# Optimization experiments

Measured on AMD Instinct MI355X. Metric: run time of the kernel, lower is better.

## Reference

```python
import jax, jax.numpy as jnp
import numpy as np

D_LATENT = 128   # per-head dim AND input embedding dim (d_q default)
N_HEADS = 16
ROPE_BASE = 10000.0


def _rope(x):
    # x: [B, H, S, D]; interleaved-pair rotary embedding over seq axis (-2)
    B, H, S, D = x.shape
    half = D // 2
    inv_freq = 1.0 / (ROPE_BASE ** (jnp.arange(half, dtype=jnp.float32) * 2.0 / D))
    ang = jnp.arange(S, dtype=jnp.float32)[:, None] * inv_freq[None, :]  # [S, half]
    cos, sin = jnp.cos(ang), jnp.sin(ang)
    xp = x.reshape(B, H, S, half, 2)
    x0, x1 = xp[..., 0], xp[..., 1]
    r0 = x0 * cos - x1 * sin
    r1 = x1 * cos + x0 * sin
    return jnp.stack([r0, r1], axis=-1).reshape(B, H, S, D)


def setup_inputs() -> dict:
    key = jax.random.key(0)
    k_q, k_wq, k_wk, k_wv, k_wo = jax.random.split(key, 5)
    B, S, E = 2, 2048, D_LATENT
    inner = N_HEADS * D_LATENT
    sc_in = 1.0 / np.sqrt(E)
    sc_inner = 1.0 / np.sqrt(inner)
    return {
        "q": jax.random.normal(k_q, (B, S, E), dtype=jnp.float32),
        "W_q": jax.random.normal(k_wq, (E, inner), dtype=jnp.float32) * sc_in,
        "W_k": jax.random.normal(k_wk, (E, inner), dtype=jnp.float32) * sc_in,
        "W_v": jax.random.normal(k_wv, (E, inner), dtype=jnp.float32) * sc_in,
        "W_o": jax.random.normal(k_wo, (inner, E), dtype=jnp.float32) * sc_inner,
    }


def reference(q, W_q, W_k, W_v, W_o):
    B, S, E = q.shape
    H, D = N_HEADS, D_LATENT
    scale = 1.0 / np.sqrt(D)
    # projections -> [B, H, S, D]
    qh = (q @ W_q).reshape(B, S, H, D).transpose(0, 2, 1, 3)
    kh = (q @ W_k).reshape(B, S, H, D).transpose(0, 2, 1, 3)
    vh = (q @ W_v).reshape(B, S, H, D).transpose(0, 2, 1, 3)
    qh = _rope(qh)
    kh = _rope(kh)
    scores = jnp.einsum("bhsd,bhtd->bhst", qh, kh) * scale  # [B,H,S,S]
    causal = jnp.tril(jnp.ones((S, S), dtype=bool))
    scores = jnp.where(causal, scores, -jnp.inf)
    probs = jax.nn.softmax(scores, axis=-1)
    out = jnp.einsum("bhst,bhtd->bhsd", probs, vh)  # [B,H,S,D]
    out = out.transpose(0, 2, 1, 3).reshape(B, S, H * D)
    return out @ W_o
```

## Files before the change

kernel.cpp:

```cpp
#include <hip/hip_runtime.h>
#include <math.h>

#define S_LEN 2048
#define NH 16
#define DH 128
#define INNER 2048
#define NROWS 4096

typedef __attribute__((ext_vector_type(8))) short bf16x8;
typedef __attribute__((ext_vector_type(4))) float f32x4;

__device__ __forceinline__ short f2bf(float f) {
  union { float f; unsigned u; } v; v.f = f;
  unsigned r = (v.u + 0x7fffu + ((v.u >> 16) & 1u)) >> 16;
  return (short)(unsigned short)r;
}
__device__ __forceinline__ float bf2f(short s) {
  union { unsigned u; float f; } v; v.u = ((unsigned)(unsigned short)s) << 16;
  return v.f;
}
__device__ __forceinline__ int pkbf(float lo, float hi) {
  union { float f; unsigned u; } x, y;
  x.f = lo; y.f = hi;
  return (int)__builtin_amdgcn_perm(y.u + 0x8000u, x.u + 0x8000u, 0x07060302u);
}
__device__ __forceinline__ void gl2lds(const short* g, short* l) {
  __builtin_amdgcn_global_load_lds(
      (const __attribute__((address_space(1))) unsigned int*)g,
      (__attribute__((address_space(3))) unsigned int*)l, 16, 0, 0);
}

__global__ void k_prep(const float* __restrict__ X, const float* __restrict__ Wq,
                       const float* __restrict__ Wk, const float* __restrict__ Wv,
                       const float* __restrict__ Wo,
                       float* __restrict__ csT, short* __restrict__ Xbf,
                       short* __restrict__ WT, short* __restrict__ WoT,
                       float* __restrict__ outz) {
  const int bx = blockIdx.x, tid = threadIdx.x;
  if (bx < 512) {
    int idx = bx * 256 + tid;
    int i = idx & 63, s = idx >> 6;
    double invf = pow(10000.0, -(double)i / 64.0);
    float ang = (float)((double)s * invf);
    float sv, cv; sincosf(ang, &sv, &cv);
    csT[idx * 2] = cv; csT[idx * 2 + 1] = sv;
    return;
  }
  if (bx < 1024) {
    int idx = ((bx - 512) * 256 + tid) * 4;
    float4 xv = *(const float4*)&X[idx];
    short4 o; o.x = f2bf(xv.x); o.y = f2bf(xv.y); o.z = f2bf(xv.z); o.w = f2bf(xv.w);
    *(short4*)&Xbf[idx] = o;
    return;
  }
  if (bx >= 2048) {
    float4 z4 = make_float4(0.f, 0.f, 0.f, 0.f);
    ((float4*)outz)[(bx - 2048) * 512 + tid] = z4;
    ((float4*)outz)[(bx - 2048) * 512 + tid + 256] = z4;
    return;
  }
  __shared__ float tile[32][33];
  const float* src; short* dst; int R, C, c0, r0;
  if (bx < 1792) {
    int z = (bx - 1024) >> 8, t = (bx - 1024) & 255;
    src = (z == 0) ? Wq : ((z == 1) ? Wk : Wv);
    dst = WT + (size_t)z * INNER * 128; R = 128; C = INNER;
    c0 = (t & 63) * 32; r0 = (t >> 6) * 32;
  } else {
    int t = bx - 1792;
    src = Wo; dst = WoT; R = INNER; C = 128;
    c0 = (t & 3) * 32; r0 = (t >> 2) * 32;
  }
  int tx = tid & 31, ty = tid >> 5;
  #pragma unroll
  for (int dy = 0; dy < 32; dy += 8)
    tile[ty + dy][tx] = src[(size_t)(r0 + ty + dy) * C + c0 + tx];
  __syncthreads();
  #pragma unroll
  for (int dy = 0; dy < 32; dy += 8)
    dst[(size_t)(c0 + ty + dy) * R + r0 + tx] = f2bf(tile[tx][ty + dy]);
}

__global__ __launch_bounds__(256, 2) void k_qkv(
    const short* __restrict__ Xbf, const short* __restrict__ WT,
    const float* __restrict__ csT,
    short* __restrict__ Qg, short* __restrict__ Kg, short* __restrict__ Vg) {
  __shared__ __attribute__((aligned(16))) short As[128 * 136];
  __shared__ __attribute__((aligned(16))) short Bs[128 * 136];
  const int tid = threadIdx.x;
  const int n0 = blockIdx.x * 128, m0 = blockIdx.y * 128;
  for (int e = tid; e < 2048; e += 256)
    *(int4*)&As[(e >> 4) * 136 + (e & 15) * 8] =
        *(const int4*)&Xbf[(size_t)(m0 + (e >> 4)) * 128 + (e & 15) * 8];
  const int wid = tid >> 6, lane = tid & 63;
  const int l16 = lane & 15, quad = lane >> 4;
  const int wm = (wid & 1) * 64, wn = (wid >> 1) * 64;
  const int hh = n0 >> 7;
  const int bb = m0 >> 11, ss = m0 & 2047;
  const float qscale = 0.12751745f;
  for (int z = 0; z < 3; ++z) {
    __syncthreads();
    const short* Wp = WT + (size_t)z * INNER * 128;
    for (int e = tid; e < 2048; e += 256)
      *(int4*)&Bs[(e >> 4) * 136 + (e & 15) * 8] =
          *(const int4*)&Wp[(size_t)(n0 + (e >> 4)) * 128 + (e & 15) * 8];
    __syncthreads();
    f32x4 acc[4][4] = {};
    #pragma unroll
    for (int ks = 0; ks < 4; ++ks) {
      bf16x8 ax[4], bw[4];
      #pragma unroll
      for (int j = 0; j < 4; ++j) {
        ax[j] = *(const bf16x8*)&As[(wm + j * 16 + l16) * 136 + ks * 32 + quad * 8];
        bw[j] = *(const bf16x8*)&Bs[(wn + j * 16 + l16) * 136 + ks * 32 + quad * 8];
      }
      if (z < 2) {
        #pragma unroll
        for (int dt = 0; dt < 4; ++dt)
          #pragma unroll
          for (int st = 0; st < 4; ++st)
            acc[dt][st] = __builtin_amdgcn_mfma_f32_16x16x32_bf16(bw[dt], ax[st], acc[dt][st], 0, 0, 0);
      } else {
        #pragma unroll
        for (int mt = 0; mt < 4; ++mt)
          #pragma unroll
          for (int nt = 0; nt < 4; ++nt)
            acc[mt][nt] = __builtin_amdgcn_mfma_f32_16x16x32_bf16(ax[mt], bw[nt], acc[mt][nt], 0, 0, 0);
      }
    }
    if (z < 2) {
      __syncthreads();
      #pragma unroll
      for (int dt = 0; dt < 4; ++dt)
        #pragma unroll
        for (int st = 0; st < 4; ++st) {
          int d0 = wn + dt * 16 + quad * 4;
          int sl = wm + st * 16 + l16;
          int sg = ss + sl;
          float4 cs = *(const float4*)&csT[((size_t)sg * 64 + (d0 >> 1)) * 2];
          float x0 = acc[dt][st][0], x1 = acc[dt][st][1];
          float x2 = acc[dt][st][2], x3 = acc[dt][st][3];
          float r0 = x0 * cs.x - x1 * cs.y, r1 = x1 * cs.x + x0 * cs.y;
          float r2 = x2 * cs.z - x3 * cs.w, r3 = x3 * cs.z + x2 * cs.w;
          if (z == 0) { r0 *= qscale; r1 *= qscale; r2 *= qscale; r3 *= qscale; }
          int2 pk; pk.x = pkbf(r0, r1); pk.y = pkbf(r2, r3);
          *(int2*)&Bs[sl * 136 + d0] = pk;
        }
      __syncthreads();
      short* dst = (z == 0 ? Qg : Kg) + (((size_t)(bb * NH + hh)) * S_LEN + ss) * DH;
      #pragma unroll
      for (int it = 0; it < 8; ++it) {
        int u = tid + 256 * it;
        int row = u >> 4, c = u & 15;
        int cc = (z == 0) ? c : (c ^ (row & 15));
        *(int4*)&dst[(size_t)row * DH + cc * 8] = *(const int4*)&Bs[row * 136 + c * 8];
      }
    } else {
      __syncthreads();
      #pragma unroll
      for (int mt = 0; mt < 4; ++mt)
        #pragma unroll
        for (int nt = 0; nt < 4; ++nt) {
          int dl = wn + nt * 16 + l16;
          int sl = wm + mt * 16 + quad * 4;
          int2 pk;
          pk.x = pkbf(acc[mt][nt][0], acc[mt][nt][1]);
          pk.y = pkbf(acc[mt][nt][2], acc[mt][nt][3]);
          *(int2*)&As[dl * 136 + sl] = pk;
        }
      __syncthreads();
      #pragma unroll
      for (int rd = 0; rd < 8; ++rd) {
        int dl = (tid >> 4) + rd * 16;
        int sl = (tid & 15) * 8;
        int tile = (ss >> 6) + (sl >> 6);
        int tl = sl & 63;
        int ch = (tl >> 3) ^ (dl & 7);
        int4 vv = *(const int4*)&As[dl * 136 + sl];
        *(int4*)&Vg[(((size_t)(bb * NH + hh) * 32 + tile) * 128 + dl) * 64 + ch * 8] = vv;
      }
    }
  }
}

__global__ __launch_bounds__(256, 2) void k_attn(
    const short* __restrict__ Qg, const short* __restrict__ Kg,
    const short* __restrict__ Vt, short* __restrict__ Op,
    float* __restrict__ mlb) {
  __shared__ __attribute__((aligned(16))) short Ks[2][64 * 128];
  __shared__ __attribute__((aligned(16))) short Vs[2][128 * 64];
  __shared__ __attribute__((aligned(16))) short Ps[4][32 * 64];
  const int bid = blockIdx.x;
  const int bh = bid & 31, unit = bid >> 5;
  const int tid = threadIdx.x, wid = tid >> 6, lane = tid & 63;
  const int l16 = lane & 15, quad = lane >> 4, wq = wid * 32;
  const float CEXP2 = 23.083121f;
  const short* Qp = Qg + (size_t)bh * S_LEN * DH;
  const short* Kp = Kg + (size_t)bh * S_LEN * DH;
  const short* Vb = Vt + (size_t)bh * 32 * 8192;
  short* psw = &Ps[wid][0];
  int kcs[4], vcs[2];
  #pragma unroll
  for (int ks = 0; ks < 4; ++ks) kcs[ks] = ((ks * 4 + quad) ^ l16) * 8;
  #pragma unroll
  for (int ks = 0; ks < 2; ++ks) vcs[ks] = ((ks * 4 + quad) ^ (l16 & 7)) * 8;

  for (int seg = 0; seg < 2; ++seg) {
    const int qg = seg ? (15 - unit) : unit;
    const int par = seg;
    const int q0 = qg * 128, nj = qg + 1;
    __syncthreads();
    {
      const short* kg = Kp + (size_t)(par * 64) * DH;
      const short* vg = Vb + (size_t)par * 8192;
      #pragma unroll
      for (int i = 0; i < 4; ++i) {
        int sl = wid * 4 + i;
        gl2lds(kg + sl * 512 + lane * 8, &Ks[0][sl * 512]);
        gl2lds(vg + sl * 512 + lane * 8, &Vs[0][sl * 512]);
      }
    }
    bf16x8 qf[4][2];
    #pragma unroll
    for (int ks = 0; ks < 4; ++ks)
      #pragma unroll
      for (int qb = 0; qb < 2; ++qb)
        qf[ks][qb] = *(const bf16x8*)&Qp[(size_t)(q0 + wq + qb * 16 + l16) * DH +
                                         ks * 32 + quad * 8];
    float l_p[2] = {0.0f, 0.0f};
    f32x4 Oacc[8][2] = {};
    for (int jj = 0; jj < nj; ++jj) {
      const int b = jj & 1;
      __syncthreads();
      if (jj + 1 < nj) {
        const int jn = par + 2 * (jj + 1);
        const short* kg = Kp + (size_t)(jn * 64) * DH;
        const short* vg = Vb + (size_t)jn * 8192;
        #pragma unroll
        for (int i = 0; i < 4; ++i) {
          int sl = wid * 4 + i;
          gl2lds(kg + sl * 512 + lane * 8, &Ks[1 - b][sl * 512]);
          gl2lds(vg + sl * 512 + lane * 8, &Vs[1 - b][sl * 512]);
        }
      }
      f32x4 Sc[4][2] = {};
      #pragma unroll
      for (int ks = 0; ks < 4; ++ks) {
        bf16x8 kfr[4];
        #pragma unroll
        for (int nt = 0; nt < 4; ++nt)
          kfr[nt] = *(const bf16x8*)&Ks[b][(nt * 16 + l16) * 128 + kcs[ks]];
        #pragma unroll
        for (int nt = 0; nt < 4; ++nt)
          #pragma unroll
          for (int qb = 0; qb < 2; ++qb)
            Sc[nt][qb] = __builtin_amdgcn_mfma_f32_16x16x32_bf16(kfr[nt], qf[ks][qb],
                                                                 Sc[nt][qb], 0, 0, 0);
      }
      const int j = par + 2 * jj;
      if (jj == nj - 1) {
        #pragma unroll
        for (int nt = 0; nt < 4; ++nt)
          #pragma unroll
          for (int qb = 0; qb < 2; ++qb)
            #pragma unroll
            for (int r = 0; r < 4; ++r) {
              int tg = j * 64 + nt * 16 + quad * 4 + r;
              int qgl = q0 + wq + qb * 16 + l16;
              if (tg > qgl) Sc[nt][qb][r] = -1000.0f;
            }
      }
      #pragma unroll
      for (int qb = 0; qb < 2; ++qb) {
        float ls0 = 0.0f, ls1 = 0.0f;
        #pragma unroll
        for (int nt = 0; nt < 4; ++nt)
          #pragma unroll
          for (int r = 0; r < 4; ++r) {
            float pe = __builtin_amdgcn_exp2f(Sc[nt][qb][r] - CEXP2);
            Sc[nt][qb][r] = pe;
            if (nt & 1) ls1 += pe; else ls0 += pe;
          }
        l_p[qb] += ls0 + ls1;
        #pragma unroll
        for (int nt = 0; nt < 4; ++nt) {
          int2 pk;
          pk.x = pkbf(Sc[nt][qb][0], Sc[nt][qb][1]);
          pk.y = pkbf(Sc[nt][qb][2], Sc[nt][qb][3]);
          int ch = ((nt * 2 + (quad >> 1)) ^ (l16 & 7)) * 8 + (quad & 1) * 4;
          *(int2*)&psw[(qb * 16 + l16) * 64 + ch] = pk;
        }
      }
      #pragma unroll
      for (int ks = 0; ks < 2; ++ks) {
        bf16x8 vfr[8];
        #pragma unroll
        for (int nt = 0; nt < 8; ++nt)
          vfr[nt] = *(const bf16x8*)&Vs[b][(nt * 16 + l16) * 64 + vcs[ks]];
        bf16x8 bp[2];
        #pragma unroll
        for (int qb = 0; qb < 2; ++qb)
          bp[qb] = *(const bf16x8*)&psw[(qb * 16 + l16) * 64 + vcs[ks]];
        #pragma unroll
        for (int nt = 0; nt < 8; ++nt)
          #pragma unroll
          for (int qb = 0; qb < 2; ++qb)
            Oacc[nt][qb] = __builtin_amdgcn_mfma_f32_16x16x32_bf16(vfr[nt], bp[qb],
                                                                   Oacc[nt][qb], 0, 0, 0);
      }
    }
    __syncthreads();
    short* osl = &Ks[0][0] + wid * 4096;
    #pragma unroll
    for (int qb = 0; qb < 2; ++qb)
      #pragma unroll
      for (int nt = 0; nt < 8; ++nt) {
        int2 ov;
        ov.x = pkbf(Oacc[nt][qb][0], Oacc[nt][qb][1]);
        ov.y = pkbf(Oacc[nt][qb][2], Oacc[nt][qb][3]);
        int ch = ((nt * 2 + (quad >> 1)) ^ l16) * 8 + (quad & 1) * 4;
        *(int2*)&osl[(qb * 16 + l16) * 128 + ch] = ov;
      }
    size_t obase = ((size_t)(par * 32 + bh) * S_LEN + q0 + wq) * DH;
    #pragma unroll
    for (int it = 0; it < 8; ++it) {
      int u = lane + 64 * it;
      int row = u >> 4, c = u & 15;
      *(int4*)&Op[obase + (size_t)row * DH + c * 8] =
          *(const int4*)&osl[row * 128 + ((c ^ (row & 15)) * 8)];
    }
    #pragma unroll
    for (int qb = 0; qb < 2; ++qb) {
      float lt = l_p[qb];
      lt += __shfl_xor(lt, 16);
      lt += __shfl_xor(lt, 32);
      int qrow = q0 + wq + qb * 16 + l16;
      if (quad == 0)
        mlb[(size_t)(par * 32 + bh) * S_LEN + qrow] = lt;
    }
  }
}

__global__ __launch_bounds__(256, 2) void k_out(
    const short* __restrict__ Op, const float* __restrict__ mlb,
    const short* __restrict__ WoT, float* __restrict__ out) {
  __shared__ __attribute__((aligned(16))) short As[32 * 136];
  __shared__ __attribute__((aligned(16))) short Bs[128 * 136];
  __shared__ float cw[4][32];
  const int m0 = blockIdx.x * 32, h0 = blockIdx.y * 4;
  const int tid = threadIdx.x, wid = tid >> 6, lane = tid & 63;
  const int l16 = lane & 15, quad = lane >> 4;
  const int wm = (wid & 1) * 16, wn = (wid >> 1) * 64;
  if (tid < 128) {
    int rr = tid & 31, hh = tid >> 5;
    int row = m0 + rr, b = row >> 11, s = row & 2047;
    int bh = b * NH + h0 + hh;
    float l1 = mlb[(size_t)bh * S_LEN + s];
    float l2 = mlb[(size_t)(32 + bh) * S_LEN + s];
    cw[hh][rr] = 1.0f / (l1 + l2);
  }
  __syncthreads();
  f32x4 acc[4] = {};
  for (int hc = 0; hc < 4; ++hc) {
    int h = h0 + hc;
    #pragma unroll
    for (int it = 0; it < 4; ++it) {
      int e = tid + 256 * it;
      int rr = e >> 5, c4 = (e & 31) * 4;
      int row = m0 + rr, b = row >> 11, s = row & 2047;
      size_t base = ((size_t)(b * NH + h) * S_LEN + s) * DH + c4;
      short4 u1 = *(const short4*)&Op[base];
      short4 u2 = *(const short4*)&Op[(size_t)32 * S_LEN * DH + base];
      float c1 = cw[hc][rr];
      int2 o;
      o.x = pkbf(c1 * (bf2f(u1.x) + bf2f(u2.x)), c1 * (bf2f(u1.y) + bf2f(u2.y)));
      o.y = pkbf(c1 * (bf2f(u1.z) + bf2f(u2.z)), c1 * (bf2f(u1.w) + bf2f(u2.w)));
      *(int2*)&As[rr * 136 + c4] = o;
    }
    for (int e = tid; e < 2048; e += 256)
      *(int4*)&Bs[(e >> 4) * 136 + (e & 15) * 8] =
          *(const int4*)&WoT[(size_t)(e >> 4) * INNER + h * 128 + (e & 15) * 8];
    __syncthreads();
    #pragma unroll
    for (int ks = 0; ks < 4; ++ks) {
      bf16x8 a = *(const bf16x8*)&As[(wm + l16) * 136 + ks * 32 + quad * 8];
      bf16x8 b[4];
      #pragma unroll
      for (int nt = 0; nt < 4; ++nt)
        b[nt] = *(const bf16x8*)&Bs[(wn + nt * 16 + l16) * 136 + ks * 32 + quad * 8];
      #pragma unroll
      for (int nt = 0; nt < 4; ++nt)
        acc[nt] = __builtin_amdgcn_mfma_f32_16x16x32_bf16(a, b[nt], acc[nt], 0, 0, 0);
    }
    __syncthreads();
  }
  #pragma unroll
  for (int nt = 0; nt < 4; ++nt)
    #pragma unroll
    for (int r = 0; r < 4; ++r) {
      int gm = m0 + wm + quad * 4 + r;
      int gn = wn + nt * 16 + l16;
      atomicAdd(&out[(size_t)gm * 128 + gn], acc[nt][r]);
    }
}

extern "C" void kernel_launch(void* const* d_in, const int* in_sizes, int n_in,
                              void* d_out, int out_size, void* d_ws, size_t ws_size,
                              hipStream_t stream) {
  const float* q  = (const float*)d_in[0];
  const float* Wq = (const float*)d_in[1];
  const float* Wk = (const float*)d_in[2];
  const float* Wv = (const float*)d_in[3];
  const float* Wo = (const float*)d_in[4];
  float* out = (float*)d_out;
  char* ws = (char*)d_ws;
  const size_t MB = 1024 * 1024;
  float* csT = (float*)(ws + 0);
  short* WT  = (short*)(ws + 1 * MB);
  short* WoT = (short*)(ws + 2 * MB + 512 * 1024);
  short* Xbf = (short*)(ws + 3 * MB);
  short* Qg  = (short*)(ws + 8 * MB);
  short* Kg  = (short*)(ws + 24 * MB);
  short* Vg  = (short*)(ws + 40 * MB);
  short* Op  = (short*)(ws + 56 * MB);
  float* mlb = (float*)(ws + 88 * MB);

  k_prep<<<2304, 256, 0, stream>>>(q, Wq, Wk, Wv, Wo, csT, Xbf, WT, WoT, out);
  k_qkv<<<dim3(16, 32), 256, 0, stream>>>(Xbf, WT, csT, Qg, Kg, Vg);
  k_attn<<<512, 256, 0, stream>>>(Qg, Kg, Vg, Op, mlb);
  k_out<<<dim3(128, 4), 256, 0, stream>>>(Op, mlb, WoT, out);
}
```

Measured before the change: 158.4 us.

## Shuffle P fragments via permlane swaps, single-buffer V, raise attention occupancy

The P tile now goes from accumulator layout into MFMA operand layout through permlane32/permlane16 swaps held in registers, so the per-wave LDS scratch buffer and its stores and loads are gone. V is single-buffered and loaded at the start of each iteration, with explicit vmcnt waits and barriers before the PV matmul. The freed LDS lets launch bounds go to 3 blocks per SM. In exchange, V load latency is now exposed inside each iteration and the register cap tightens, which could cause spills.

New measurement: 169.1 us. 1.07x slower.

```diff
diff --git a/kernel.cpp b/kernel.cpp
--- a/kernel.cpp
+++ b/kernel.cpp
@@ -9,6 +9,7 @@
 
 typedef __attribute__((ext_vector_type(8))) short bf16x8;
 typedef __attribute__((ext_vector_type(4))) float f32x4;
+typedef __attribute__((ext_vector_type(2))) unsigned int u32x2;
 
 __device__ __forceinline__ short f2bf(float f) {
   union { float f; unsigned u; } v; v.f = f;
@@ -28,6 +29,14 @@
   __builtin_amdgcn_global_load_lds(
       (const __attribute__((address_space(1))) unsigned int*)g,
       (__attribute__((address_space(3))) unsigned int*)l, 16, 0, 0);
+}
+__device__ __forceinline__ void pl32swap(int& a, int& b) {
+  u32x2 r = __builtin_amdgcn_permlane32_swap((unsigned)a, (unsigned)b, false, false);
+  a = (int)r.x; b = (int)r.y;
+}
+__device__ __forceinline__ void pl16swap(int& a, int& b) {
+  u32x2 r = __builtin_amdgcn_permlane16_swap((unsigned)a, (unsigned)b, false, false);
+  a = (int)r.x; b = (int)r.y;
 }
 
 __global__ void k_prep(const float* __restrict__ X, const float* __restrict__ Wq,
@@ -183,13 +192,12 @@
   }
 }
 
-__global__ __launch_bounds__(256, 2) void k_attn(
+__global__ __launch_bounds__(256, 3) void k_attn(
     const short* __restrict__ Qg, const short* __restrict__ Kg,
     const short* __restrict__ Vt, short* __restrict__ Op,
     float* __restrict__ mlb) {
   __shared__ __attribute__((aligned(16))) short Ks[2][64 * 128];
-  __shared__ __attribute__((aligned(16))) short Vs[2][128 * 64];
-  __shared__ __attribute__((aligned(16))) short Ps[4][32 * 64];
+  __shared__ __attribute__((aligned(16))) short Vs[64 * 128];
   const int bid = blockIdx.x;
   const int bh = bid & 31, unit = bid >> 5;
   const int tid = threadIdx.x, wid = tid >> 6, lane = tid & 63;
@@ -198,7 +206,6 @@
   const short* Qp = Qg + (size_t)bh * S_LEN * DH;
   const short* Kp = Kg + (size_t)bh * S_LEN * DH;
   const short* Vb = Vt + (size_t)bh * 32 * 8192;
-  short* psw = &Ps[wid][0];
   int kcs[4], vcs[2];
   #pragma unroll
   for (int ks = 0; ks < 4; ++ks) kcs[ks] = ((ks * 4 + quad) ^ l16) * 8;
@@ -212,12 +219,10 @@
     __syncthreads();
     {
       const short* kg = Kp + (size_t)(par * 64) * DH;
-      const short* vg = Vb + (size_t)par * 8192;
       #pragma unroll
       for (int i = 0; i < 4; ++i) {
         int sl = wid * 4 + i;
         gl2lds(kg + sl * 512 + lane * 8, &Ks[0][sl * 512]);
-        gl2lds(vg + sl * 512 + lane * 8, &Vs[0][sl * 512]);
       }
     }
     bf16x8 qf[4][2];
@@ -231,16 +236,26 @@
     f32x4 Oacc[8][2] = {};
     for (int jj = 0; jj < nj; ++jj) {
       const int b = jj & 1;
-      __syncthreads();
-      if (jj + 1 < nj) {
+      const int j = par + 2 * jj;
+      asm volatile("s_waitcnt vmcnt(0)" ::: "memory");
+      __builtin_amdgcn_s_barrier();
+      __builtin_amdgcn_sched_barrier(0);
+      {
+        const short* vg = Vb + (size_t)j * 8192;
+        #pragma unroll
+        for (int i = 0; i < 4; ++i) {
+          int sl = wid * 4 + i;
+          gl2lds(vg + sl * 512 + lane * 8, &Vs[sl * 512]);
+        }
+      }
+      const int havek = (jj + 1 < nj);
+      if (havek) {
         const int jn = par + 2 * (jj + 1);
         const short* kg = Kp + (size_t)(jn * 64) * DH;
-        const short* vg = Vb + (size_t)jn * 8192;
         #pragma unroll
         for (int i = 0; i < 4; ++i) {
           int sl = wid * 4 + i;
           gl2lds(kg + sl * 512 + lane * 8, &Ks[1 - b][sl * 512]);
-          gl2lds(vg + sl * 512 + lane * 8, &Vs[1 - b][sl * 512]);
         }
       }
       f32x4 Sc[4][2] = {};
@@ -257,7 +272,6 @@
             Sc[nt][qb] = __builtin_amdgcn_mfma_f32_16x16x32_bf16(kfr[nt], qf[ks][qb],
                                                                  Sc[nt][qb], 0, 0, 0);
       }
-      const int j = par + 2 * jj;
       if (jj == nj - 1) {
         #pragma unroll
         for (int nt = 0; nt < 4; ++nt)
@@ -270,6 +284,7 @@
               if (tg > qgl) Sc[nt][qb][r] = -1000.0f;
             }
       }
+      bf16x8 bpf[2][2];
       #pragma unroll
       for (int qb = 0; qb < 2; ++qb) {
         float ls0 = 0.0f, ls1 = 0.0f;
@@ -282,30 +297,36 @@
             if (nt & 1) ls1 += pe; else ls0 += pe;
           }
         l_p[qb] += ls0 + ls1;
+        int px[4], py[4];
         #pragma unroll
         for (int nt = 0; nt < 4; ++nt) {
-          int2 pk;
-          pk.x = pkbf(Sc[nt][qb][0], Sc[nt][qb][1]);
-          pk.y = pkbf(Sc[nt][qb][2], Sc[nt][qb][3]);
-          int ch = ((nt * 2 + (quad >> 1)) ^ (l16 & 7)) * 8 + (quad & 1) * 4;
-          *(int2*)&psw[(qb * 16 + l16) * 64 + ch] = pk;
+          px[nt] = pkbf(Sc[nt][qb][0], Sc[nt][qb][1]);
+          py[nt] = pkbf(Sc[nt][qb][2], Sc[nt][qb][3]);
         }
-      }
+        pl32swap(px[0], px[1]); pl16swap(px[0], px[1]);
+        pl32swap(py[0], py[1]); pl16swap(py[0], py[1]);
+        pl32swap(px[2], px[3]); pl16swap(px[2], px[3]);
+        pl32swap(py[2], py[3]); pl16swap(py[2], py[3]);
+        union { int i[4]; bf16x8 v; } u0, u1;
+        u0.i[0] = px[0]; u0.i[1] = py[0]; u0.i[2] = px[1]; u0.i[3] = py[1];
+        u1.i[0] = px[2]; u1.i[1] = py[2]; u1.i[2] = px[3]; u1.i[3] = py[3];
+        bpf[qb][0] = u0.v; bpf[qb][1] = u1.v;
+      }
+      if (havek) asm volatile("s_waitcnt vmcnt(4)" ::: "memory");
+      else       asm volatile("s_waitcnt vmcnt(0)" ::: "memory");
+      __builtin_amdgcn_s_barrier();
+      __builtin_amdgcn_sched_barrier(0);
       #pragma unroll
       for (int ks = 0; ks < 2; ++ks) {
         bf16x8 vfr[8];
         #pragma unroll
         for (int nt = 0; nt < 8; ++nt)
-          vfr[nt] = *(const bf16x8*)&Vs[b][(nt * 16 + l16) * 64 + vcs[ks]];
-        bf16x8 bp[2];
-        #pragma unroll
-        for (int qb = 0; qb < 2; ++qb)
-          bp[qb] = *(const bf16x8*)&psw[(qb * 16 + l16) * 64 + vcs[ks]];
+          vfr[nt] = *(const bf16x8*)&Vs[(nt * 16 + l16) * 64 + vcs[ks]];
         #pragma unroll
         for (int nt = 0; nt < 8; ++nt)
           #pragma unroll
           for (int qb = 0; qb < 2; ++qb)
-            Oacc[nt][qb] = __builtin_amdgcn_mfma_f32_16x16x32_bf16(vfr[nt], bp[qb],
+            Oacc[nt][qb] = __builtin_amdgcn_mfma_f32_16x16x32_bf16(vfr[nt], bpf[qb][ks],
                                                                    Oacc[nt][qb], 0, 0, 0);
       }
     }
```
